# Optimization experiments

Hardware: AMD Instinct MI355X
Metric: run time of the kernel (lower is better)

The kernel has to match this reference:

```python
import jax, jax.numpy as jnp
import numpy as np
import math

B, S, D, H = 4, 2048, 1024, 16
HD = D // H
WINDOW = 86400.0 * 7.0  # 7 days, per create_time_mask(window_size=...)


def setup_inputs() -> dict:
    key = jax.random.key(0)
    ks = jax.random.split(key, 12)
    x = jax.random.normal(ks[0], (B, S, D), dtype=jnp.float32)
    # transaction timestamps: uniform over 30 days, sorted per sequence
    timestamps = jnp.sort(jax.random.uniform(ks[1], (B, S), dtype=jnp.float32) * (86400.0 * 30.0), axis=-1)
    init = 0.02
    Wq = jax.random.normal(ks[2], (D, D), dtype=jnp.float32) * init
    bq = jnp.zeros((D,), dtype=jnp.float32)
    Wk = jax.random.normal(ks[3], (D, D), dtype=jnp.float32) * init
    bk = jnp.zeros((D,), dtype=jnp.float32)
    Wv = jax.random.normal(ks[4], (D, D), dtype=jnp.float32) * init
    bv = jnp.zeros((D,), dtype=jnp.float32)
    Wo = jax.random.normal(ks[5], (D, D), dtype=jnp.float32) * init
    bo = jnp.zeros((D,), dtype=jnp.float32)
    Wc = jax.random.normal(ks[6], (1, D), dtype=jnp.float32) * init
    bc = jnp.zeros((1,), dtype=jnp.float32)
    return {"x": x, "timestamps": timestamps, "Wq": Wq, "bq": bq, "Wk": Wk, "bk": bk,
            "Wv": Wv, "bv": bv, "Wo": Wo, "bo": bo, "Wc": Wc, "bc": bc}


def reference(x, timestamps, Wq, bq, Wk, bk, Wv, bv, Wo, bo, Wc, bc):
    b, s, d = x.shape
    scale = 1.0 / math.sqrt(HD)
    # projections (torch Linear: y = x @ W.T + b), split heads -> [b, s, H, HD]
    Q = (x @ Wq.T + bq).reshape(b, s, H, HD)
    K = (x @ Wk.T + bk).reshape(b, s, H, HD)
    V = (x @ Wv.T + bv).reshape(b, s, H, HD)
    # scores [b, H, q, k]
    scores = jnp.einsum('bqhd,bkhd->bhqk', Q, K) * scale
    # time-window mask: attend only within +/- WINDOW seconds
    time_mask = jnp.abs(timestamps[:, :, None] - timestamps[:, None, :]) <= WINDOW  # [b, s, s]
    scores = jnp.where(time_mask[:, None, :, :], scores, -jnp.inf)
    attn = jax.nn.softmax(scores, axis=-1)
    attended = jnp.einsum('bhqk,bkhd->bqhd', attn, V).reshape(b, s, d)
    output = attended @ Wo.T + bo
    change_scores = (output @ Wc.T + bc)[..., 0]  # [b, s]
    return output, change_scores
```

## Files before the change

kernel.cpp:

```cpp
#include <hip/hip_runtime.h>
#include <math.h>

#define BB 4
#define SS 2048
#define DD 1024
#define HH 16
#define HDD 64
#define NN (BB*SS)
#define WINDOWF 604800.0f
#define LOG2E 1.44269504088896340736f
#define SCALE2 (0.125f * LOG2E)

typedef __attribute__((ext_vector_type(8))) short bf16x8;
typedef __attribute__((ext_vector_type(4))) short bf16x4;
typedef __attribute__((ext_vector_type(4))) short s16x4;
typedef __attribute__((ext_vector_type(4))) float f32x4;

__device__ __forceinline__ unsigned short f2b(float f) {
    unsigned int x = __float_as_uint(f);
    unsigned int r = x + 0x7FFFu + ((x >> 16) & 1u);
    return (unsigned short)(r >> 16);
}

__device__ __forceinline__ unsigned int cvt_pk_bf16(float lo, float hi) {
    unsigned int r;
    asm("v_cvt_pk_bf16_f32 %0, %1, %2" : "=v"(r) : "v"(lo), "v"(hi));
    return r;
}

__device__ __forceinline__ void gload16(const unsigned short* g, unsigned short* l) {
    __builtin_amdgcn_global_load_lds(
        (const __attribute__((address_space(1))) unsigned int*)g,
        (__attribute__((address_space(3))) unsigned int*)l, 16, 0, 0);
}

__global__ __launch_bounds__(256)
void cvt_band(const float* __restrict__ x,
              const float* __restrict__ Wq, const float* __restrict__ Wk,
              const float* __restrict__ Wv, const float* __restrict__ Wo,
              const float* __restrict__ ts,
              unsigned short* __restrict__ xb,
              unsigned short* __restrict__ Wqb, unsigned short* __restrict__ Wkb,
              unsigned short* __restrict__ Wvb, unsigned short* __restrict__ Wob,
              int* __restrict__ lo, int* __restrict__ hi)
{
    const int g = blockIdx.x;
    const int tid = threadIdx.x;
    if (g < 12288) {
        const float* src; unsigned short* dst; int i;
        if (g < 8192) { src = x; dst = xb; i = g * 1024 + tid * 4; }
        else {
            const int wi = (g - 8192) >> 10;
            src = (wi == 0) ? Wq : (wi == 1) ? Wk : (wi == 2) ? Wv : Wo;
            dst = (wi == 0) ? Wqb : (wi == 1) ? Wkb : (wi == 2) ? Wvb : Wob;
            i = ((g - 8192) & 1023) * 1024 + tid * 4;
        }
        float4 v = *(const float4*)(src + i);
        s16x4 o;
        o[0] = (short)f2b(v.x); o[1] = (short)f2b(v.y);
        o[2] = (short)f2b(v.z); o[3] = (short)f2b(v.w);
        *(s16x4*)(dst + i) = o;
    } else {
        const int idx = (g - 12288) * 256 + tid;
        const int b = idx / SS, q = idx % SS;
        const float* t = ts + (size_t)b * SS;
        float tq = t[q];
        float lot = tq - WINDOWF - 1.0f;
        float hit = tq + WINDOWF + 1.0f;
        int l = 0, r = q;
        while (l < r) { int m = (l + r) >> 1; if (t[m] < lot) l = m + 1; else r = m; }
        lo[idx] = l;
        int l2 = q, r2 = SS - 1;
        while (l2 < r2) { int m = (l2 + r2 + 1) >> 1; if (t[m] > hit) r2 = m - 1; else l2 = m; }
        hi[idx] = l2;
    }
}

template<int OUTMODE>
__global__ __launch_bounds__(256)
void gemm_bf16(const unsigned short* __restrict__ A,
               const unsigned short* __restrict__ Bw,
               const float* __restrict__ bias,
               void* __restrict__ Y, int M, int N, int K, float alpha)
{
    constexpr int BM = 128, BN = 128, BK = 64;
    __shared__ unsigned short As[BM * BK];
    __shared__ unsigned short Bs[BN * BK];

    const int bm = blockIdx.x * BM;
    const int bn = blockIdx.y * BN;
    const int tid = threadIdx.x;
    const int wid = tid >> 6, l = tid & 63;
    const int wm = (wid >> 1) * 64, wn = (wid & 1) * 64;
    const int lr = l & 15, lg = l >> 4;

    const int srow = l >> 3;
    const int schunk = ((l & 7) ^ srow) * 8;

    f32x4 acc[4][4];
#pragma unroll
    for (int i = 0; i < 4; ++i)
#pragma unroll
        for (int j = 0; j < 4; ++j) acc[i][j] = (f32x4){0.f, 0.f, 0.f, 0.f};

    for (int k0 = 0; k0 < K; k0 += BK) {
#pragma unroll
        for (int i = 0; i < 4; ++i) {
            const int r0 = wid * 32 + i * 8;
            gload16(A  + (size_t)(bm + r0 + srow) * K + k0 + schunk, &As[r0 * BK]);
            gload16(Bw + (size_t)(bn + r0 + srow) * K + k0 + schunk, &Bs[r0 * BK]);
        }
        __syncthreads();

#pragma unroll
        for (int ks = 0; ks < 2; ++ks) {
            bf16x8 af[4], bf[4];
#pragma unroll
            for (int am = 0; am < 4; ++am) {
                const int row = wm + am * 16 + lr;
                af[am] = *(const bf16x8*)&As[row * BK + (((ks * 4 + lg) ^ (row & 7)) * 8)];
            }
#pragma unroll
            for (int nf = 0; nf < 4; ++nf) {
                const int row = wn + nf * 16 + lr;
                bf[nf] = *(const bf16x8*)&Bs[row * BK + (((ks * 4 + lg) ^ (row & 7)) * 8)];
            }
#pragma unroll
            for (int am = 0; am < 4; ++am)
#pragma unroll
                for (int nf = 0; nf < 4; ++nf)
                    acc[am][nf] = __builtin_amdgcn_mfma_f32_16x16x32_bf16(
                        af[am], bf[nf], acc[am][nf], 0, 0, 0);
        }
        __syncthreads();
    }

    float bia[4];
#pragma unroll
    for (int nf = 0; nf < 4; ++nf) bia[nf] = bias[bn + wn + nf * 16 + lr];

#pragma unroll
    for (int am = 0; am < 4; ++am)
#pragma unroll
        for (int nf = 0; nf < 4; ++nf) {
            if (OUTMODE == 2) {
                int mbase = bm + wm + am * 16 + lg * 4;
                int n = bn + wn + nf * 16 + lr;
                int bidx = mbase >> 11, sidx = mbase & (SS - 1);
                s16x4 o;
#pragma unroll
                for (int r = 0; r < 4; ++r)
                    o[r] = (short)f2b((acc[am][nf][r] + bia[nf]) * alpha);
                *(s16x4*)((unsigned short*)Y +
                          (((size_t)(bidx << 10) + n) << 11) + sidx) = o;
            } else {
#pragma unroll
                for (int r = 0; r < 4; ++r) {
                    float o = (acc[am][nf][r] + bia[nf]) * alpha;
                    size_t m = (size_t)(bm + wm + am * 16 + lg * 4 + r);
                    size_t n = (size_t)(bn + wn + nf * 16 + lr);
                    if (OUTMODE == 1) ((unsigned short*)Y)[m * N + n] = f2b(o);
                    else              ((float*)Y)[m * N + n] = o;
                }
            }
        }
}

__global__ __launch_bounds__(256)
void attn_mfma(const unsigned short* __restrict__ Qb, const unsigned short* __restrict__ Kb,
               const unsigned short* __restrict__ Vt, const float* __restrict__ Tg,
               const int* __restrict__ lo, const int* __restrict__ hi,
               unsigned short* __restrict__ Ab)
{
    __shared__ unsigned short Ks[2][64 * 64];
    __shared__ unsigned short Vs[2][64 * 64];

    const int blk = blockIdx.x;
    const int xcd = blk & 7;
    const int idx = blk >> 3;
    const int bh  = xcd * 8 + (idx >> 5);
    const int qt  = idx & 31;
    const int b = bh >> 4, h = bh & 15;

    const int tid = threadIdx.x;
    const int wid = tid >> 6, l = tid & 63;
    const int lr = l & 15, lg = l >> 4;
    const int q0w = qt * 64 + wid * 16;

    const size_t qrow = (size_t)(b * SS + q0w + lr);
    const bf16x8 qf0 = *(const bf16x8*)(Qb + qrow * DD + h * HDD + lg * 8);
    const bf16x8 qf1 = *(const bf16x8*)(Qb + qrow * DD + h * HDD + 32 + lg * 8);

    const float* tb = Tg + (size_t)b * SS;
    const float tq = tb[q0w + lr];
    const float tq_min = tb[qt * 64];
    const float tq_max = tb[qt * 64 + 63];

    const int t0 = lo[b * SS + qt * 64] >> 6;
    const int t1 = hi[b * SS + qt * 64 + 63] >> 6;

    const unsigned short* Kbh = Kb + (size_t)b * SS * DD + h * HDD;
    const unsigned short* Vth = Vt + ((size_t)(b * 1024 + h * HDD)) * SS;

    const int srow = l >> 3;
    const int schunk = (((l & 7) - srow) & 7) * 8;

    const unsigned short* kg0 = Kbh + (size_t)(t0 * 64 + wid * 16 + srow) * DD + schunk;
    const unsigned short* kg1 = kg0 + 8 * DD;
    const unsigned short* vg0 = Vth + (size_t)(wid * 16 + srow) * SS + t0 * 64 + schunk;
    const unsigned short* vg1 = vg0 + 8 * SS;

    const int ka_off = lr * 64 + (((lg + lr) & 7) << 3);
    const int c0 = lg >> 1, h4 = (lg & 1) * 4;
    const int pv0 = lr * 64 + (((c0 + 0 + lr) & 7) << 3) + h4;
    const int pv1 = lr * 64 + (((c0 + 2 + lr) & 7) << 3) + h4;
    const int pv2 = lr * 64 + (((c0 + 4 + lr) & 7) << 3) + h4;
    const int pv3 = lr * 64 + (((c0 + 6 + lr) & 7) << 3) + h4;

    unsigned short *Kc = &Ks[0][0], *Kn = &Ks[1][0];
    unsigned short *Vc = &Vs[0][0], *Vn = &Vs[1][0];

    float m_ = -1e30f, l_ = 0.f;
    f32x4 o_[4];
#pragma unroll
    for (int df = 0; df < 4; ++df) o_[df] = (f32x4){0.f, 0.f, 0.f, 0.f};

    gload16(kg0, Kc + wid * 1024);
    gload16(kg1, Kc + wid * 1024 + 512);
    gload16(vg0, Vc + wid * 1024);
    gload16(vg1, Vc + wid * 1024 + 512);
    kg0 += 64 * DD; kg1 += 64 * DD; vg0 += 64; vg1 += 64;
    __syncthreads();

    for (int t = t0; t <= t1; ++t) {
        const int kk0 = t * 64;

        if (t < t1) {
            gload16(kg0, Kn + wid * 1024);
            gload16(kg1, Kn + wid * 1024 + 512);
            gload16(vg0, Vn + wid * 1024);
            gload16(vg1, Vn + wid * 1024 + 512);
            kg0 += 64 * DD; kg1 += 64 * DD; vg0 += 64; vg1 += 64;
        }

        f32x4 s[4];
        __builtin_amdgcn_s_setprio(1);
#pragma unroll
        for (int kf = 0; kf < 4; ++kf) {
            bf16x8 ka0 = *(const bf16x8*)(Kc + kf * 1024 + ka_off);
            bf16x8 ka1 = *(const bf16x8*)(Kc + kf * 1024 + (ka_off ^ 32));
            f32x4 z = (f32x4){0.f, 0.f, 0.f, 0.f};
            z = __builtin_amdgcn_mfma_f32_16x16x32_bf16(ka0, qf0, z, 0, 0, 0);
            z = __builtin_amdgcn_mfma_f32_16x16x32_bf16(ka1, qf1, z, 0, 0, 0);
            s[kf] = z;
        }
        __builtin_amdgcn_s_setprio(0);

        const bool needmask = !((tq_max - tb[kk0] <= WINDOWF - 4.0f) &&
                                (tb[kk0 + 63] - tq_min <= WINDOWF - 4.0f));
        if (needmask) {
#pragma unroll
            for (int kf = 0; kf < 4; ++kf) {
                float4 tk4 = *(const float4*)(tb + kk0 + kf * 16 + lg * 4);
                if (!(fabsf(tq - tk4.x) <= WINDOWF)) s[kf][0] = -INFINITY;
                if (!(fabsf(tq - tk4.y) <= WINDOWF)) s[kf][1] = -INFINITY;
                if (!(fabsf(tq - tk4.z) <= WINDOWF)) s[kf][2] = -INFINITY;
                if (!(fabsf(tq - tk4.w) <= WINDOWF)) s[kf][3] = -INFINITY;
            }
        }

        float t1_ = fmaxf(fmaxf(s[0][0], s[0][1]), s[0][2]);
        float t2_ = fmaxf(fmaxf(s[0][3], s[1][0]), s[1][1]);
        float t3_ = fmaxf(fmaxf(s[1][2], s[1][3]), s[2][0]);
        float t4_ = fmaxf(fmaxf(s[2][1], s[2][2]), s[2][3]);
        float t5_ = fmaxf(fmaxf(s[3][0], s[3][1]), s[3][2]);
        float mt = fmaxf(fmaxf(fmaxf(t1_, t2_), fmaxf(t3_, t4_)),
                         fmaxf(t5_, s[3][3]));
        mt = fmaxf(mt, __shfl_xor(mt, 16));
        mt = fmaxf(mt, __shfl_xor(mt, 32));
        if (!__all(mt <= m_ + 8.0f)) {
            const float mn = fmaxf(m_, mt);
            const float f_ = __builtin_amdgcn_exp2f(m_ - mn);
            l_ *= f_;
#pragma unroll
            for (int df = 0; df < 4; ++df)
#pragma unroll
                for (int r = 0; r < 4; ++r) o_[df][r] *= f_;
            m_ = mn;
        }
        float rs = 0.f;
#pragma unroll
        for (int kf = 0; kf < 4; ++kf)
#pragma unroll
            for (int r = 0; r < 4; ++r) {
                float p = __builtin_amdgcn_exp2f(s[kf][r] - m_);
                s[kf][r] = p;
                rs += p;
            }
        rs += __shfl_xor(rs, 16);
        rs += __shfl_xor(rs, 32);
        l_ += rs;

        union { unsigned int u[4]; bf16x8 v; } pb[2];
#pragma unroll
        for (int c = 0; c < 2; ++c) {
            pb[c].u[0] = cvt_pk_bf16(s[2 * c][0],     s[2 * c][1]);
            pb[c].u[1] = cvt_pk_bf16(s[2 * c][2],     s[2 * c][3]);
            pb[c].u[2] = cvt_pk_bf16(s[2 * c + 1][0], s[2 * c + 1][1]);
            pb[c].u[3] = cvt_pk_bf16(s[2 * c + 1][2], s[2 * c + 1][3]);
        }

        __builtin_amdgcn_s_setprio(1);
#pragma unroll
        for (int df = 0; df < 4; ++df) {
            const int base = df * 1024;
            union { bf16x4 hh[2]; bf16x8 v; } va0, va1;
            va0.hh[0] = *(const bf16x4*)(Vc + base + pv0);
            va0.hh[1] = *(const bf16x4*)(Vc + base + pv1);
            va1.hh[0] = *(const bf16x4*)(Vc + base + pv2);
            va1.hh[1] = *(const bf16x4*)(Vc + base + pv3);
            o_[df] = __builtin_amdgcn_mfma_f32_16x16x32_bf16(va0.v, pb[0].v, o_[df], 0, 0, 0);
            o_[df] = __builtin_amdgcn_mfma_f32_16x16x32_bf16(va1.v, pb[1].v, o_[df], 0, 0, 0);
        }
        __builtin_amdgcn_s_setprio(0);

        __syncthreads();
        unsigned short* tk = Kc; Kc = Kn; Kn = tk;
        unsigned short* tv = Vc; Vc = Vn; Vn = tv;
    }

    const float inv = 1.f / l_;
#pragma unroll
    for (int df = 0; df < 4; ++df) {
        s16x4 o;
#pragma unroll
        for (int r = 0; r < 4; ++r) o[r] = (short)f2b(o_[df][r] * inv);
        *(s16x4*)(Ab + qrow * DD + h * HDD + df * 16 + lg * 4) = o;
    }
}

__global__ __launch_bounds__(256)
void change_kernel(const float* __restrict__ out, const float* __restrict__ Wc,
                   const float* __restrict__ bc, float* __restrict__ cs)
{
    int row = blockIdx.x * 4 + (threadIdx.x >> 6);
    int lane = threadIdx.x & 63;
    const float* o = out + (size_t)row * DD;
    float sum = 0.f;
#pragma unroll
    for (int k = 0; k < DD / 256; ++k) {
        int c = lane * 4 + k * 256;
        float4 v = *(const float4*)(o + c);
        float4 w = *(const float4*)(Wc + c);
        sum += v.x * w.x + v.y * w.y + v.z * w.z + v.w * w.w;
    }
#pragma unroll
    for (int off = 1; off < 64; off <<= 1) sum += __shfl_xor(sum, off);
    if (lane == 0) cs[row] = sum + bc[0];
}

extern "C" void kernel_launch(void* const* d_in, const int* in_sizes, int n_in,
                              void* d_out, int out_size, void* d_ws, size_t ws_size,
                              hipStream_t stream)
{
    (void)in_sizes; (void)n_in; (void)out_size; (void)ws_size;
    const float* x  = (const float*)d_in[0];
    const float* ts = (const float*)d_in[1];
    const float* Wq = (const float*)d_in[2];
    const float* bq = (const float*)d_in[3];
    const float* Wk = (const float*)d_in[4];
    const float* bk = (const float*)d_in[5];
    const float* Wv = (const float*)d_in[6];
    const float* bv = (const float*)d_in[7];
    const float* Wo = (const float*)d_in[8];
    const float* bo = (const float*)d_in[9];
    const float* Wc = (const float*)d_in[10];
    const float* bc = (const float*)d_in[11];

    float* out = (float*)d_out;

    unsigned short* xb  = (unsigned short*)d_ws;
    unsigned short* Qb  = xb  + (size_t)NN * DD;
    unsigned short* Kb2 = Qb  + (size_t)NN * DD;
    unsigned short* Vtb = Kb2 + (size_t)NN * DD;
    unsigned short* Abf = Vtb + (size_t)NN * DD;
    unsigned short* Wqb = Abf + (size_t)NN * DD;
    unsigned short* Wkb = Wqb + (size_t)DD * DD;
    unsigned short* Wvb = Wkb + (size_t)DD * DD;
    unsigned short* Wob = Wvb + (size_t)DD * DD;
    int* lo = (int*)(Wob + (size_t)DD * DD);
    int* hi = lo + NN;

    cvt_band<<<12320, 256, 0, stream>>>(x, Wq, Wk, Wv, Wo, ts,
                                        xb, Wqb, Wkb, Wvb, Wob, lo, hi);

    dim3 g(NN / 128, DD / 128);
    gemm_bf16<1><<<g, 256, 0, stream>>>(xb, Wqb, bq, Qb,  NN, DD, DD, SCALE2);
    gemm_bf16<1><<<g, 256, 0, stream>>>(xb, Wkb, bk, Kb2, NN, DD, DD, 1.0f);
    gemm_bf16<2><<<g, 256, 0, stream>>>(xb, Wvb, bv, Vtb, NN, DD, DD, 1.0f);
    attn_mfma<<<BB * HH * (SS / 64), 256, 0, stream>>>(Qb, Kb2, Vtb, ts, lo, hi, Abf);
    gemm_bf16<0><<<g, 256, 0, stream>>>(Abf, Wob, bo, out, NN, DD, DD, 1.0f);
    change_kernel<<<NN / 4, 256, 0, stream>>>(out, Wc, bc, out + (size_t)NN * DD);
}
```

Measured before the change: 196.9 us.

## Process two 16-row query groups per wave to reuse K/V tiles

Doubles the attention query tile from 64 to 128 rows per block, with each wave computing two independent 16-row softmax/accumulate streams against the same shared-memory K/V tiles. This halves the number of blocks and the K/V global-to-LDS traffic per query, and amortizes LDS fragment reads across two MFMA chains. In exchange it raises register pressure and widens the key band each block scans, since the band bounds now come from 128 queries.

```diff
diff --git a/kernel.cpp b/kernel.cpp
--- a/kernel.cpp
+++ b/kernel.cpp
@@ -178,26 +178,31 @@
     const int blk = blockIdx.x;
     const int xcd = blk & 7;
     const int idx = blk >> 3;
-    const int bh  = xcd * 8 + (idx >> 5);
-    const int qt  = idx & 31;
+    const int bh  = xcd * 8 + (idx >> 4);
+    const int qt  = idx & 15;
     const int b = bh >> 4, h = bh & 15;
 
     const int tid = threadIdx.x;
     const int wid = tid >> 6, l = tid & 63;
     const int lr = l & 15, lg = l >> 4;
-    const int q0w = qt * 64 + wid * 16;
-
-    const size_t qrow = (size_t)(b * SS + q0w + lr);
-    const bf16x8 qf0 = *(const bf16x8*)(Qb + qrow * DD + h * HDD + lg * 8);
-    const bf16x8 qf1 = *(const bf16x8*)(Qb + qrow * DD + h * HDD + 32 + lg * 8);
+    const int qA = qt * 128 + wid * 32;
+    const int qB = qA + 16;
+
+    const size_t rowA = (size_t)(b * SS + qA + lr);
+    const size_t rowB = (size_t)(b * SS + qB + lr);
+    const bf16x8 qfA0 = *(const bf16x8*)(Qb + rowA * DD + h * HDD + lg * 8);
+    const bf16x8 qfA1 = *(const bf16x8*)(Qb + rowA * DD + h * HDD + 32 + lg * 8);
+    const bf16x8 qfB0 = *(const bf16x8*)(Qb + rowB * DD + h * HDD + lg * 8);
+    const bf16x8 qfB1 = *(const bf16x8*)(Qb + rowB * DD + h * HDD + 32 + lg * 8);
 
     const float* tb = Tg + (size_t)b * SS;
-    const float tq = tb[q0w + lr];
-    const float tq_min = tb[qt * 64];
-    const float tq_max = tb[qt * 64 + 63];
-
-    const int t0 = lo[b * SS + qt * 64] >> 6;
-    const int t1 = hi[b * SS + qt * 64 + 63] >> 6;
+    const float tqA = tb[qA + lr];
+    const float tqB = tb[qB + lr];
+    const float tq_min = tb[qA];
+    const float tq_max = tb[qB + 15];
+
+    const int t0 = lo[b * SS + qt * 128] >> 6;
+    const int t1 = hi[b * SS + qt * 128 + 127] >> 6;
 
     const unsigned short* Kbh = Kb + (size_t)b * SS * DD + h * HDD;
     const unsigned short* Vth = Vt + ((size_t)(b * 1024 + h * HDD)) * SS;
@@ -220,10 +225,13 @@
     unsigned short *Kc = &Ks[0][0], *Kn = &Ks[1][0];
     unsigned short *Vc = &Vs[0][0], *Vn = &Vs[1][0];
 
-    float m_ = -1e30f, l_ = 0.f;
-    f32x4 o_[4];
-#pragma unroll
-    for (int df = 0; df < 4; ++df) o_[df] = (f32x4){0.f, 0.f, 0.f, 0.f};
+    float mA = -1e30f, lA = 0.f, mB = -1e30f, lB = 0.f;
+    f32x4 oA[4], oB[4];
+#pragma unroll
+    for (int df = 0; df < 4; ++df) {
+        oA[df] = (f32x4){0.f, 0.f, 0.f, 0.f};
+        oB[df] = (f32x4){0.f, 0.f, 0.f, 0.f};
+    }
 
     gload16(kg0, Kc + wid * 1024);
     gload16(kg1, Kc + wid * 1024 + 512);
@@ -243,16 +251,20 @@
             kg0 += 64 * DD; kg1 += 64 * DD; vg0 += 64; vg1 += 64;
         }
 
-        f32x4 s[4];
+        f32x4 sA[4], sB[4];
         __builtin_amdgcn_s_setprio(1);
 #pragma unroll
         for (int kf = 0; kf < 4; ++kf) {
             bf16x8 ka0 = *(const bf16x8*)(Kc + kf * 1024 + ka_off);
             bf16x8 ka1 = *(const bf16x8*)(Kc + kf * 1024 + (ka_off ^ 32));
-            f32x4 z = (f32x4){0.f, 0.f, 0.f, 0.f};
-            z = __builtin_amdgcn_mfma_f32_16x16x32_bf16(ka0, qf0, z, 0, 0, 0);
-            z = __builtin_amdgcn_mfma_f32_16x16x32_bf16(ka1, qf1, z, 0, 0, 0);
-            s[kf] = z;
+            f32x4 zA = (f32x4){0.f, 0.f, 0.f, 0.f};
+            zA = __builtin_amdgcn_mfma_f32_16x16x32_bf16(ka0, qfA0, zA, 0, 0, 0);
+            zA = __builtin_amdgcn_mfma_f32_16x16x32_bf16(ka1, qfA1, zA, 0, 0, 0);
+            sA[kf] = zA;
+            f32x4 zB = (f32x4){0.f, 0.f, 0.f, 0.f};
+            zB = __builtin_amdgcn_mfma_f32_16x16x32_bf16(ka0, qfB0, zB, 0, 0, 0);
+            zB = __builtin_amdgcn_mfma_f32_16x16x32_bf16(ka1, qfB1, zB, 0, 0, 0);
+            sB[kf] = zB;
         }
         __builtin_amdgcn_s_setprio(0);
 
@@ -262,52 +274,95 @@
 #pragma unroll
             for (int kf = 0; kf < 4; ++kf) {
                 float4 tk4 = *(const float4*)(tb + kk0 + kf * 16 + lg * 4);
-                if (!(fabsf(tq - tk4.x) <= WINDOWF)) s[kf][0] = -INFINITY;
-                if (!(fabsf(tq - tk4.y) <= WINDOWF)) s[kf][1] = -INFINITY;
-                if (!(fabsf(tq - tk4.z) <= WINDOWF)) s[kf][2] = -INFINITY;
-                if (!(fabsf(tq - tk4.w) <= WINDOWF)) s[kf][3] = -INFINITY;
-            }
-        }
-
-        float t1_ = fmaxf(fmaxf(s[0][0], s[0][1]), s[0][2]);
-        float t2_ = fmaxf(fmaxf(s[0][3], s[1][0]), s[1][1]);
-        float t3_ = fmaxf(fmaxf(s[1][2], s[1][3]), s[2][0]);
-        float t4_ = fmaxf(fmaxf(s[2][1], s[2][2]), s[2][3]);
-        float t5_ = fmaxf(fmaxf(s[3][0], s[3][1]), s[3][2]);
-        float mt = fmaxf(fmaxf(fmaxf(t1_, t2_), fmaxf(t3_, t4_)),
-                         fmaxf(t5_, s[3][3]));
-        mt = fmaxf(mt, __shfl_xor(mt, 16));
-        mt = fmaxf(mt, __shfl_xor(mt, 32));
-        if (!__all(mt <= m_ + 8.0f)) {
-            const float mn = fmaxf(m_, mt);
-            const float f_ = __builtin_amdgcn_exp2f(m_ - mn);
-            l_ *= f_;
-#pragma unroll
-            for (int df = 0; df < 4; ++df)
-#pragma unroll
-                for (int r = 0; r < 4; ++r) o_[df][r] *= f_;
-            m_ = mn;
-        }
-        float rs = 0.f;
-#pragma unroll
-        for (int kf = 0; kf < 4; ++kf)
-#pragma unroll
-            for (int r = 0; r < 4; ++r) {
-                float p = __builtin_amdgcn_exp2f(s[kf][r] - m_);
-                s[kf][r] = p;
-                rs += p;
-            }
-        rs += __shfl_xor(rs, 16);
-        rs += __shfl_xor(rs, 32);
-        l_ += rs;
-
-        union { unsigned int u[4]; bf16x8 v; } pb[2];
+                if (!(fabsf(tqA - tk4.x) <= WINDOWF)) sA[kf][0] = -INFINITY;
+                if (!(fabsf(tqA - tk4.y) <= WINDOWF)) sA[kf][1] = -INFINITY;
+                if (!(fabsf(tqA - tk4.z) <= WINDOWF)) sA[kf][2] = -INFINITY;
+                if (!(fabsf(tqA - tk4.w) <= WINDOWF)) sA[kf][3] = -INFINITY;
+                if (!(fabsf(tqB - tk4.x) <= WINDOWF)) sB[kf][0] = -INFINITY;
+                if (!(fabsf(tqB - tk4.y) <= WINDOWF)) sB[kf][1] = -INFINITY;
+                if (!(fabsf(tqB - tk4.z) <= WINDOWF)) sB[kf][2] = -INFINITY;
+                if (!(fabsf(tqB - tk4.w) <= WINDOWF)) sB[kf][3] = -INFINITY;
+            }
+        }
+
+        {
+            float u1 = fmaxf(fmaxf(sA[0][0], sA[0][1]), sA[0][2]);
+            float u2 = fmaxf(fmaxf(sA[0][3], sA[1][0]), sA[1][1]);
+            float u3 = fmaxf(fmaxf(sA[1][2], sA[1][3]), sA[2][0]);
+            float u4 = fmaxf(fmaxf(sA[2][1], sA[2][2]), sA[2][3]);
+            float u5 = fmaxf(fmaxf(sA[3][0], sA[3][1]), sA[3][2]);
+            float mt = fmaxf(fmaxf(fmaxf(u1, u2), fmaxf(u3, u4)),
+                             fmaxf(u5, sA[3][3]));
+            mt = fmaxf(mt, __shfl_xor(mt, 16));
+            mt = fmaxf(mt, __shfl_xor(mt, 32));
+            if (!__all(mt <= mA + 8.0f)) {
+                const float mn = fmaxf(mA, mt);
+                const float f_ = __builtin_amdgcn_exp2f(mA - mn);
+                lA *= f_;
+#pragma unroll
+                for (int df = 0; df < 4; ++df)
+#pragma unroll
+                    for (int r = 0; r < 4; ++r) oA[df][r] *= f_;
+                mA = mn;
+            }
+            float rs = 0.f;
+#pragma unroll
+            for (int kf = 0; kf < 4; ++kf)
+#pragma unroll
+                for (int r = 0; r < 4; ++r) {
+                    float p = __builtin_amdgcn_exp2f(sA[kf][r] - mA);
+                    sA[kf][r] = p;
+                    rs += p;
+                }
+            rs += __shfl_xor(rs, 16);
+            rs += __shfl_xor(rs, 32);
+            lA += rs;
+        }
+        {
+            float u1 = fmaxf(fmaxf(sB[0][0], sB[0][1]), sB[0][2]);
+            float u2 = fmaxf(fmaxf(sB[0][3], sB[1][0]), sB[1][1]);
+            float u3 = fmaxf(fmaxf(sB[1][2], sB[1][3]), sB[2][0]);
+            float u4 = fmaxf(fmaxf(sB[2][1], sB[2][2]), sB[2][3]);
+            float u5 = fmaxf(fmaxf(sB[3][0], sB[3][1]), sB[3][2]);
+            float mt = fmaxf(fmaxf(fmaxf(u1, u2), fmaxf(u3, u4)),
+                             fmaxf(u5, sB[3][3]));
+            mt = fmaxf(mt, __shfl_xor(mt, 16));
+            mt = fmaxf(mt, __shfl_xor(mt, 32));
+            if (!__all(mt <= mB + 8.0f)) {
+                const float mn = fmaxf(mB, mt);
+                const float f_ = __builtin_amdgcn_exp2f(mB - mn);
+                lB *= f_;
+#pragma unroll
+                for (int df = 0; df < 4; ++df)
+#pragma unroll
+                    for (int r = 0; r < 4; ++r) oB[df][r] *= f_;
+                mB = mn;
+            }
+            float rs = 0.f;
+#pragma unroll
+            for (int kf = 0; kf < 4; ++kf)
+#pragma unroll
+                for (int r = 0; r < 4; ++r) {
+                    float p = __builtin_amdgcn_exp2f(sB[kf][r] - mB);
+                    sB[kf][r] = p;
+                    rs += p;
+                }
+            rs += __shfl_xor(rs, 16);
+            rs += __shfl_xor(rs, 32);
+            lB += rs;
+        }
+
+        union { unsigned int u[4]; bf16x8 v; } pbA[2], pbB[2];
 #pragma unroll
         for (int c = 0; c < 2; ++c) {
-            pb[c].u[0] = cvt_pk_bf16(s[2 * c][0],     s[2 * c][1]);
-            pb[c].u[1] = cvt_pk_bf16(s[2 * c][2],     s[2 * c][3]);
-            pb[c].u[2] = cvt_pk_bf16(s[2 * c + 1][0], s[2 * c + 1][1]);
-            pb[c].u[3] = cvt_pk_bf16(s[2 * c + 1][2], s[2 * c + 1][3]);
+            pbA[c].u[0] = cvt_pk_bf16(sA[2 * c][0],     sA[2 * c][1]);
+            pbA[c].u[1] = cvt_pk_bf16(sA[2 * c][2],     sA[2 * c][3]);
+            pbA[c].u[2] = cvt_pk_bf16(sA[2 * c + 1][0], sA[2 * c + 1][1]);
+            pbA[c].u[3] = cvt_pk_bf16(sA[2 * c + 1][2], sA[2 * c + 1][3]);
+            pbB[c].u[0] = cvt_pk_bf16(sB[2 * c][0],     sB[2 * c][1]);
+            pbB[c].u[1] = cvt_pk_bf16(sB[2 * c][2],     sB[2 * c][3]);
+            pbB[c].u[2] = cvt_pk_bf16(sB[2 * c + 1][0], sB[2 * c + 1][1]);
+            pbB[c].u[3] = cvt_pk_bf16(sB[2 * c + 1][2], sB[2 * c + 1][3]);
         }
 
         __builtin_amdgcn_s_setprio(1);
@@ -319,8 +374,10 @@
             va0.hh[1] = *(const bf16x4*)(Vc + base + pv1);
             va1.hh[0] = *(const bf16x4*)(Vc + base + pv2);
             va1.hh[1] = *(const bf16x4*)(Vc + base + pv3);
-            o_[df] = __builtin_amdgcn_mfma_f32_16x16x32_bf16(va0.v, pb[0].v, o_[df], 0, 0, 0);
-            o_[df] = __builtin_amdgcn_mfma_f32_16x16x32_bf16(va1.v, pb[1].v, o_[df], 0, 0, 0);
+            oA[df] = __builtin_amdgcn_mfma_f32_16x16x32_bf16(va0.v, pbA[0].v, oA[df], 0, 0, 0);
+            oA[df] = __builtin_amdgcn_mfma_f32_16x16x32_bf16(va1.v, pbA[1].v, oA[df], 0, 0, 0);
+            oB[df] = __builtin_amdgcn_mfma_f32_16x16x32_bf16(va0.v, pbB[0].v, oB[df], 0, 0, 0);
+            oB[df] = __builtin_amdgcn_mfma_f32_16x16x32_bf16(va1.v, pbB[1].v, oB[df], 0, 0, 0);
         }
         __builtin_amdgcn_s_setprio(0);
 
@@ -329,13 +386,17 @@
         unsigned short* tv = Vc; Vc = Vn; Vn = tv;
     }
 
-    const float inv = 1.f / l_;
+    const float invA = 1.f / lA, invB = 1.f / lB;
 #pragma unroll
     for (int df = 0; df < 4; ++df) {
-        s16x4 o;
-#pragma unroll
-        for (int r = 0; r < 4; ++r) o[r] = (short)f2b(o_[df][r] * inv);
-        *(s16x4*)(Ab + qrow * DD + h * HDD + df * 16 + lg * 4) = o;
+        s16x4 a, bo_;
+#pragma unroll
+        for (int r = 0; r < 4; ++r) {
+            a[r]   = (short)f2b(oA[df][r] * invA);
+            bo_[r] = (short)f2b(oB[df][r] * invB);
+        }
+        *(s16x4*)(Ab + rowA * DD + h * HDD + df * 16 + lg * 4) = a;
+        *(s16x4*)(Ab + rowB * DD + h * HDD + df * 16 + lg * 4) = bo_;
     }
 }
 
@@ -398,7 +459,7 @@
     gemm_bf16<1><<<g, 256, 0, stream>>>(xb, Wqb, bq, Qb,  NN, DD, DD, SCALE2);
     gemm_bf16<1><<<g, 256, 0, stream>>>(xb, Wkb, bk, Kb2, NN, DD, DD, 1.0f);
     gemm_bf16<2><<<g, 256, 0, stream>>>(xb, Wvb, bv, Vtb, NN, DD, DD, 1.0f);
-    attn_mfma<<<BB * HH * (SS / 64), 256, 0, stream>>>(Qb, Kb2, Vtb, ts, lo, hi, Abf);
+    attn_mfma<<<BB * HH * (SS / 128), 256, 0, stream>>>(Qb, Kb2, Vtb, ts, lo, hi, Abf);
     gemm_bf16<0><<<g, 256, 0, stream>>>(Abf, Wob, bo, out, NN, DD, DD, 1.0f);
     change_kernel<<<NN / 4, 256, 0, stream>>>(out, Wc, bc, out + (size_t)NN * DD);
 }
```

Result: slower. 205.3 us (+4.2%).
